# Kernel tuning notes

Hardware: AMD Instinct MI355X
Metric: run time of the kernel (lower is better)

The kernel has to match this reference:

```python
import jax, jax.numpy as jnp
import numpy as np

L1 = 1536
L2 = 15
L3 = 64
COUNT = 8
B = 16384


def setup_inputs() -> dict:
    key = jax.random.key(0)
    ks = jax.random.split(key, 10)
    d_in = 2 * L1 // 2  # 1536
    s1 = 1.0 / np.sqrt(d_in)
    s2 = 1.0 / np.sqrt(2 * L2)
    s3 = 1.0 / np.sqrt(L3)
    return {
        "x": jax.random.normal(ks[0], (B, d_in), dtype=jnp.float32),
        "ls_indices": jax.random.randint(ks[1], (B,), 0, COUNT, dtype=jnp.int32),
        "W1": jax.random.uniform(ks[2], (COUNT * (L2 + 1), d_in), jnp.float32, -s1, s1),
        "b1": jax.random.uniform(ks[3], (COUNT * (L2 + 1),), jnp.float32, -s1, s1),
        "Wf": jax.random.uniform(ks[4], (L2 + 1, d_in), jnp.float32, -s1, s1),
        "bf": jax.random.uniform(ks[5], (L2 + 1,), jnp.float32, -s1, s1),
        "W2": jax.random.uniform(ks[6], (COUNT * L3, 2 * L2), jnp.float32, -s2, s2),
        "b2": jax.random.uniform(ks[7], (COUNT * L3,), jnp.float32, -s2, s2),
        "Wo": jax.random.uniform(ks[8], (COUNT, L3), jnp.float32, -s3, s3),
        "bo": jax.random.uniform(ks[9], (COUNT,), jnp.float32, -s3, s3),
    }


def reference(x, ls_indices, W1, b1, Wf, bf, W2, b2, Wo, bo):
    count = Wo.shape[0]
    n = x.shape[0]
    idx = ls_indices[:, None, None]  # [B,1,1] selects the per-sample stack

    # l1: all stacks, then gather selected stack row per sample
    l1s = (x @ W1.T + b1).reshape(n, count, L2 + 1)          # [B, count, 16]
    l1f = x @ Wf.T + bf                                       # [B, 16]
    l1c = jnp.take_along_axis(l1s, idx, axis=1)[:, 0]         # [B, 16]

    l1c_, l1c_out = l1c[:, :L2], l1c[:, L2:]                  # [B,15], [B,1]
    l1f_, l1f_out = l1f[:, :L2], l1f[:, L2:]
    l1x = l1c_ + l1f_
    # squared-clipped-ReLU concat: [pow(x,2)*127/128, x] clamped to [0,1]
    l1x = jnp.clip(jnp.concatenate([l1x * l1x * (127.0 / 128.0), l1x], axis=1), 0.0, 1.0)  # [B,30]

    l2s = (l1x @ W2.T + b2).reshape(n, count, L3)             # [B, count, 64]
    l2c = jnp.take_along_axis(l2s, idx, axis=1)[:, 0]         # [B, 64]
    l2x = jnp.clip(l2c, 0.0, 1.0)

    l3s = (l2x @ Wo.T + bo).reshape(n, count, 1)              # [B, count, 1]
    l3c = jnp.take_along_axis(l3s, idx, axis=1)[:, 0]         # [B, 1]
    return l3c + l1f_out + l1c_out
```

## Files before the change

kernel.cpp:

```cpp
#include <hip/hip_runtime.h>
#include <hip/hip_bf16.h>
#include <stdint.h>

#define L1DIM 1536
#define NOUT  144
#define BK    64
#define MTILE 32
#define NCHUNK16 1152

typedef __bf16 bf16;
typedef __bf16 bf16x8 __attribute__((ext_vector_type(8)));
typedef float  floatx4 __attribute__((ext_vector_type(4)));

__global__ void pack_weights(const float* __restrict__ W1,
                             const float* __restrict__ Wf,
                             bf16* __restrict__ pw) {
    int t = blockIdx.x * blockDim.x + threadIdx.x;
    if (t >= 192 * NOUT) return;
    int o = t / NOUT;
    int n = t % NOUT;
    const float* src = (n < 128) ? (W1 + (size_t)n * L1DIM + o * 8)
                                 : (Wf + (size_t)(n - 128) * L1DIM + o * 8);
    bf16* dst = pw + (size_t)t * 8;
#pragma unroll
    for (int j = 0; j < 8; j++) dst[j] = (bf16)src[j];
}

__device__ __forceinline__ void gload_lds16(const void* g, void* l) {
    __builtin_amdgcn_global_load_lds(
        (const __attribute__((address_space(1))) void*)g,
        (__attribute__((address_space(3))) void*)l, 16, 0, 0);
}

__global__ __launch_bounds__(256) void layerstacks_main(
    const float* __restrict__ x, const int* __restrict__ lsidx,
    const bf16* __restrict__ pw,
    const float* __restrict__ b1, const float* __restrict__ bf_,
    const float* __restrict__ W2, const float* __restrict__ b2,
    const float* __restrict__ Wo, const float* __restrict__ bo,
    float* __restrict__ out)
{
    __shared__ bf16  lb[8 * NOUT * 8];
    __shared__ float ep[MTILE][148];

    const int tid  = threadIdx.x;
    const int wv   = tid >> 6;
    const int ln   = tid & 63;
    const int quad = ln >> 4;
    const int lm   = ln & 15;

    const int R0  = blockIdx.x * MTILE;
    const int ms  = wv & 1;
    const int nh  = wv >> 1;
    const int nt0 = nh ? 5 : 0;
    const int ntn = nh ? 4 : 5;

    const float* xrow = x + (size_t)(R0 + ms * 16 + lm) * L1DIM;

    floatx4 acc[5];
#pragma unroll
    for (int i = 0; i < 5; i++) acc[i] = (floatx4){0.f, 0.f, 0.f, 0.f};

    for (int ki = 0; ki < L1DIM / BK; ki++) {
        const int k0 = ki * BK;
        __syncthreads();
        {
            const bf16* src = pw + (size_t)(k0 / 8) * NOUT * 8;
            for (int base = wv * 64; base < NCHUNK16; base += 256) {
                gload_lds16(src + (size_t)(base + ln) * 8, &lb[(size_t)base * 8 + ln * 8]);
            }
        }
        float4 a0 = *(const float4*)(xrow + k0 + quad * 8);
        float4 a1 = *(const float4*)(xrow + k0 + quad * 8 + 4);
        float4 a2 = *(const float4*)(xrow + k0 + 32 + quad * 8);
        float4 a3 = *(const float4*)(xrow + k0 + 32 + quad * 8 + 4);
        bf16x8 af0, af1;
        {
            float t0[8] = {a0.x, a0.y, a0.z, a0.w, a1.x, a1.y, a1.z, a1.w};
            float t1[8] = {a2.x, a2.y, a2.z, a2.w, a3.x, a3.y, a3.z, a3.w};
#pragma unroll
            for (int j = 0; j < 8; j++) { af0[j] = (bf16)t0[j]; af1[j] = (bf16)t1[j]; }
        }
        __syncthreads();
#pragma unroll
        for (int t = 0; t < 5; t++) {
            if (t < ntn) {
                const int nt = nt0 + t;
                bf16x8 bf0 = *(const bf16x8*)&lb[((quad)     * NOUT + nt * 16 + lm) * 8];
                bf16x8 bf1 = *(const bf16x8*)&lb[((4 + quad) * NOUT + nt * 16 + lm) * 8];
                acc[t] = __builtin_amdgcn_mfma_f32_16x16x32_bf16(af0, bf0, acc[t], 0, 0, 0);
                acc[t] = __builtin_amdgcn_mfma_f32_16x16x32_bf16(af1, bf1, acc[t], 0, 0, 0);
            }
        }
    }

#pragma unroll
    for (int t = 0; t < 5; t++) {
        if (t < ntn) {
            const int nt = nt0 + t;
#pragma unroll
            for (int r = 0; r < 4; r++)
                ep[ms * 16 + quad * 4 + r][nt * 16 + lm] = acc[t][r];
        }
    }
    __syncthreads();

    const int er   = tid >> 3;
    const int sub  = tid & 7;
    const int grow = R0 + er;
    const int bkt  = lsidx[grow];

    const float l1c15 = ep[er][bkt * 16 + 15] + b1[bkt * 16 + 15];
    const float l1f15 = ep[er][128 + 15] + bf_[15];

    float l1x[30];
#pragma unroll
    for (int j = 0; j < 15; j++) {
        float tj = (ep[er][bkt * 16 + j] + b1[bkt * 16 + j])
                 + (ep[er][128 + j]      + bf_[j]);
        float sq = tj * tj * (127.0f / 128.0f);
        l1x[j]      = fminf(fmaxf(sq, 0.f), 1.f);
        l1x[15 + j] = fminf(fmaxf(tj, 0.f), 1.f);
    }

    float part = 0.f;
#pragma unroll
    for (int o = 0; o < 8; o++) {
        const int oi = bkt * 64 + sub * 8 + o;
        const float2* wrow = (const float2*)(W2 + oi * 30);
        float a = b2[oi];
#pragma unroll
        for (int j2 = 0; j2 < 15; j2++) {
            float2 w = wrow[j2];
            a += l1x[2 * j2] * w.x + l1x[2 * j2 + 1] * w.y;
        }
        a = fminf(fmaxf(a, 0.f), 1.f);
        part += a * Wo[oi];
    }
    part += __shfl_xor(part, 1);
    part += __shfl_xor(part, 2);
    part += __shfl_xor(part, 4);
    if (sub == 0) out[grow] = part + bo[bkt] + l1c15 + l1f15;
}

extern "C" void kernel_launch(void* const* d_in, const int* in_sizes, int n_in,
                              void* d_out, int out_size, void* d_ws, size_t ws_size,
                              hipStream_t stream) {
    const float* x   = (const float*)d_in[0];
    const int*   idx = (const int*)  d_in[1];
    const float* W1  = (const float*)d_in[2];
    const float* b1  = (const float*)d_in[3];
    const float* Wf  = (const float*)d_in[4];
    const float* bf  = (const float*)d_in[5];
    const float* W2  = (const float*)d_in[6];
    const float* b2  = (const float*)d_in[7];
    const float* Wo  = (const float*)d_in[8];
    const float* bo  = (const float*)d_in[9];
    float* out = (float*)d_out;
    bf16*  pw  = (bf16*)d_ws;

    pack_weights<<<dim3((192 * NOUT + 255) / 256), dim3(256), 0, stream>>>(W1, Wf, pw);
    layerstacks_main<<<dim3(16384 / MTILE), dim3(256), 0, stream>>>(
        x, idx, pw, b1, bf, W2, b2, Wo, bo, out);
}
```

Measured before the change: 186.6 us.

## Split K across waves, read packed weights from global, drop LDS staging

The main GEMM loop no longer stages weight tiles into LDS with per-iteration barriers. Each wave pair now takes half of the K dimension and computes all 9 N-tiles, reading B fragments straight from global/L2. The two halves are reduced through the epilogue shared buffer. The pack kernel now reads float4 and writes vectors with a transposed thread mapping for coalesced reads. The trade is more global/L2 weight traffic per block and more accumulator registers, in exchange for removing the barriers and the LDS copy.

```diff
diff --git a/kernel.cpp b/kernel.cpp
--- a/kernel.cpp
+++ b/kernel.cpp
@@ -4,9 +4,8 @@
 
 #define L1DIM 1536
 #define NOUT  144
-#define BK    64
 #define MTILE 32
-#define NCHUNK16 1152
+#define KHALF 24
 
 typedef __bf16 bf16;
 typedef __bf16 bf16x8 __attribute__((ext_vector_type(8)));
@@ -16,20 +15,17 @@
                              const float* __restrict__ Wf,
                              bf16* __restrict__ pw) {
     int t = blockIdx.x * blockDim.x + threadIdx.x;
-    if (t >= 192 * NOUT) return;
-    int o = t / NOUT;
-    int n = t % NOUT;
+    if (t >= NOUT * 192) return;
+    int n = t / 192;
+    int o = t % 192;
     const float* src = (n < 128) ? (W1 + (size_t)n * L1DIM + o * 8)
                                  : (Wf + (size_t)(n - 128) * L1DIM + o * 8);
-    bf16* dst = pw + (size_t)t * 8;
-#pragma unroll
-    for (int j = 0; j < 8; j++) dst[j] = (bf16)src[j];
-}
-
-__device__ __forceinline__ void gload_lds16(const void* g, void* l) {
-    __builtin_amdgcn_global_load_lds(
-        (const __attribute__((address_space(1))) void*)g,
-        (__attribute__((address_space(3))) void*)l, 16, 0, 0);
+    float4 s0 = ((const float4*)src)[0];
+    float4 s1 = ((const float4*)src)[1];
+    bf16x8 v;
+    v[0] = (bf16)s0.x; v[1] = (bf16)s0.y; v[2] = (bf16)s0.z; v[3] = (bf16)s0.w;
+    v[4] = (bf16)s1.x; v[5] = (bf16)s1.y; v[6] = (bf16)s1.z; v[7] = (bf16)s1.w;
+    *(bf16x8*)(pw + ((size_t)o * NOUT + n) * 8) = v;
 }
 
 __global__ __launch_bounds__(256) void layerstacks_main(
@@ -40,7 +36,6 @@
     const float* __restrict__ Wo, const float* __restrict__ bo,
     float* __restrict__ out)
 {
-    __shared__ bf16  lb[8 * NOUT * 8];
     __shared__ float ep[MTILE][148];
 
     const int tid  = threadIdx.x;
@@ -49,59 +44,47 @@
     const int quad = ln >> 4;
     const int lm   = ln & 15;
 
-    const int R0  = blockIdx.x * MTILE;
-    const int ms  = wv & 1;
-    const int nh  = wv >> 1;
-    const int nt0 = nh ? 5 : 0;
-    const int ntn = nh ? 4 : 5;
+    const int R0 = blockIdx.x * MTILE;
+    const int ms = wv & 1;
+    const int kh = wv >> 1;
 
-    const float* xrow = x + (size_t)(R0 + ms * 16 + lm) * L1DIM;
+    const float* xrow = x + (size_t)(R0 + ms * 16 + lm) * L1DIM + kh * (KHALF * 32);
+    const bf16* pwb = pw + ((size_t)(kh * 96 + quad) * NOUT + lm) * 8;
 
-    floatx4 acc[5];
+    floatx4 acc[9];
 #pragma unroll
-    for (int i = 0; i < 5; i++) acc[i] = (floatx4){0.f, 0.f, 0.f, 0.f};
+    for (int i = 0; i < 9; i++) acc[i] = (floatx4){0.f, 0.f, 0.f, 0.f};
 
-    for (int ki = 0; ki < L1DIM / BK; ki++) {
-        const int k0 = ki * BK;
-        __syncthreads();
-        {
-            const bf16* src = pw + (size_t)(k0 / 8) * NOUT * 8;
-            for (int base = wv * 64; base < NCHUNK16; base += 256) {
-                gload_lds16(src + (size_t)(base + ln) * 8, &lb[(size_t)base * 8 + ln * 8]);
-            }
-        }
-        float4 a0 = *(const float4*)(xrow + k0 + quad * 8);
-        float4 a1 = *(const float4*)(xrow + k0 + quad * 8 + 4);
-        float4 a2 = *(const float4*)(xrow + k0 + 32 + quad * 8);
-        float4 a3 = *(const float4*)(xrow + k0 + 32 + quad * 8 + 4);
-        bf16x8 af0, af1;
-        {
-            float t0[8] = {a0.x, a0.y, a0.z, a0.w, a1.x, a1.y, a1.z, a1.w};
-            float t1[8] = {a2.x, a2.y, a2.z, a2.w, a3.x, a3.y, a3.z, a3.w};
+#pragma unroll 3
+    for (int s = 0; s < KHALF; s++) {
+        float4 a0 = *(const float4*)(xrow + s * 32 + quad * 8);
+        float4 a1 = *(const float4*)(xrow + s * 32 + quad * 8 + 4);
+        bf16x8 af;
+        af[0] = (bf16)a0.x; af[1] = (bf16)a0.y; af[2] = (bf16)a0.z; af[3] = (bf16)a0.w;
+        af[4] = (bf16)a1.x; af[5] = (bf16)a1.y; af[6] = (bf16)a1.z; af[7] = (bf16)a1.w;
+
+        const bf16* bb = pwb + (size_t)s * 4 * NOUT * 8;
 #pragma unroll
-            for (int j = 0; j < 8; j++) { af0[j] = (bf16)t0[j]; af1[j] = (bf16)t1[j]; }
-        }
-        __syncthreads();
-#pragma unroll
-        for (int t = 0; t < 5; t++) {
-            if (t < ntn) {
-                const int nt = nt0 + t;
-                bf16x8 bf0 = *(const bf16x8*)&lb[((quad)     * NOUT + nt * 16 + lm) * 8];
-                bf16x8 bf1 = *(const bf16x8*)&lb[((4 + quad) * NOUT + nt * 16 + lm) * 8];
-                acc[t] = __builtin_amdgcn_mfma_f32_16x16x32_bf16(af0, bf0, acc[t], 0, 0, 0);
-                acc[t] = __builtin_amdgcn_mfma_f32_16x16x32_bf16(af1, bf1, acc[t], 0, 0, 0);
-            }
+        for (int nt = 0; nt < 9; nt++) {
+            bf16x8 bfrag = *(const bf16x8*)(bb + nt * 16 * 8);
+            acc[nt] = __builtin_amdgcn_mfma_f32_16x16x32_bf16(af, bfrag, acc[nt], 0, 0, 0);
         }
     }
 
+    if (kh == 0) {
 #pragma unroll
-    for (int t = 0; t < 5; t++) {
-        if (t < ntn) {
-            const int nt = nt0 + t;
+        for (int nt = 0; nt < 9; nt++)
 #pragma unroll
             for (int r = 0; r < 4; r++)
-                ep[ms * 16 + quad * 4 + r][nt * 16 + lm] = acc[t][r];
-        }
+                ep[ms * 16 + quad * 4 + r][nt * 16 + lm] = acc[nt][r];
+    }
+    __syncthreads();
+    if (kh == 1) {
+#pragma unroll
+        for (int nt = 0; nt < 9; nt++)
+#pragma unroll
+            for (int r = 0; r < 4; r++)
+                ep[ms * 16 + quad * 4 + r][nt * 16 + lm] += acc[nt][r];
     }
     __syncthreads();
 
@@ -159,7 +142,7 @@
     float* out = (float*)d_out;
     bf16*  pw  = (bf16*)d_ws;
 
-    pack_weights<<<dim3((192 * NOUT + 255) / 256), dim3(256), 0, stream>>>(W1, Wf, pw);
+    pack_weights<<<dim3((NOUT * 192 + 255) / 256), dim3(256), 0, stream>>>(W1, Wf, pw);
     layerstacks_main<<<dim3(16384 / MTILE), dim3(256), 0, stream>>>(
         x, idx, pw, b1, bf, W2, b2, Wo, bo, out);
 }
```

After: 225.1 us. +20.7%, slower.

## Double-buffer weight tiles in LDS, prefetch x, and double rows per block

Applied to the files above, without the earlier changes.

The main GEMM loop now double-buffers the packed weight tile in LDS and prefetches the next x slice into registers while the MFMAs work on the current one. This leaves one barrier per iteration instead of two and overlaps global loads with compute. The block grows to 512 threads covering 64 rows, so each weight tile loaded into LDS is reused across twice as many rows. The pack kernel is also reworked to read source rows contiguously with float4 loads and write 16-byte vectors. The cost is double the LDS for weights and a larger epilogue buffer, which may lower occupancy.

```diff
diff --git a/kernel.cpp b/kernel.cpp
--- a/kernel.cpp
+++ b/kernel.cpp
@@ -4,8 +4,9 @@
 
 #define L1DIM 1536
 #define NOUT  144
+#define MTILE 64
 #define BK    64
-#define MTILE 32
+#define NITER (L1DIM / BK)
 #define NCHUNK16 1152
 
 typedef __bf16 bf16;
@@ -16,14 +17,17 @@
                              const float* __restrict__ Wf,
                              bf16* __restrict__ pw) {
     int t = blockIdx.x * blockDim.x + threadIdx.x;
-    if (t >= 192 * NOUT) return;
-    int o = t / NOUT;
-    int n = t % NOUT;
+    if (t >= NOUT * 192) return;
+    int n = t / 192;
+    int o = t % 192;
     const float* src = (n < 128) ? (W1 + (size_t)n * L1DIM + o * 8)
                                  : (Wf + (size_t)(n - 128) * L1DIM + o * 8);
-    bf16* dst = pw + (size_t)t * 8;
-#pragma unroll
-    for (int j = 0; j < 8; j++) dst[j] = (bf16)src[j];
+    float4 s0 = ((const float4*)src)[0];
+    float4 s1 = ((const float4*)src)[1];
+    bf16x8 v;
+    v[0] = (bf16)s0.x; v[1] = (bf16)s0.y; v[2] = (bf16)s0.z; v[3] = (bf16)s0.w;
+    v[4] = (bf16)s1.x; v[5] = (bf16)s1.y; v[6] = (bf16)s1.z; v[7] = (bf16)s1.w;
+    *(bf16x8*)(pw + ((size_t)o * NOUT + n) * 8) = v;
 }
 
 __device__ __forceinline__ void gload_lds16(const void* g, void* l) {
@@ -32,7 +36,7 @@
         (__attribute__((address_space(3))) void*)l, 16, 0, 0);
 }
 
-__global__ __launch_bounds__(256) void layerstacks_main(
+__global__ __launch_bounds__(512) void layerstacks_main(
     const float* __restrict__ x, const int* __restrict__ lsidx,
     const bf16* __restrict__ pw,
     const float* __restrict__ b1, const float* __restrict__ bf_,
@@ -40,7 +44,7 @@
     const float* __restrict__ Wo, const float* __restrict__ bo,
     float* __restrict__ out)
 {
-    __shared__ bf16  lb[8 * NOUT * 8];
+    __shared__ bf16  lb[2][8 * NOUT * 8];
     __shared__ float ep[MTILE][148];
 
     const int tid  = threadIdx.x;
@@ -50,48 +54,61 @@
     const int lm   = ln & 15;
 
     const int R0  = blockIdx.x * MTILE;
-    const int ms  = wv & 1;
-    const int nh  = wv >> 1;
+    const int rg  = wv & 3;
+    const int nh  = wv >> 2;
     const int nt0 = nh ? 5 : 0;
     const int ntn = nh ? 4 : 5;
 
-    const float* xrow = x + (size_t)(R0 + ms * 16 + lm) * L1DIM;
+    const float* xrow = x + (size_t)(R0 + rg * 16 + lm) * L1DIM;
 
     floatx4 acc[5];
 #pragma unroll
     for (int i = 0; i < 5; i++) acc[i] = (floatx4){0.f, 0.f, 0.f, 0.f};
 
-    for (int ki = 0; ki < L1DIM / BK; ki++) {
-        const int k0 = ki * BK;
-        __syncthreads();
-        {
-            const bf16* src = pw + (size_t)(k0 / 8) * NOUT * 8;
-            for (int base = wv * 64; base < NCHUNK16; base += 256) {
-                gload_lds16(src + (size_t)(base + ln) * 8, &lb[(size_t)base * 8 + ln * 8]);
+#pragma unroll
+    for (int c = 0; c < 3; c++) {
+        int ch = tid + c * 512;
+        if (ch < NCHUNK16) gload_lds16(pw + (size_t)ch * 8, &lb[0][(size_t)ch * 8]);
+    }
+    float4 a0 = *(const float4*)(xrow + quad * 8);
+    float4 a1 = *(const float4*)(xrow + quad * 8 + 4);
+    float4 a2 = *(const float4*)(xrow + 32 + quad * 8);
+    float4 a3 = *(const float4*)(xrow + 32 + quad * 8 + 4);
+    __syncthreads();
+
+    for (int ki = 0; ki < NITER; ki++) {
+        const int cur = ki & 1;
+        if (ki < NITER - 1) {
+            const bf16* src = pw + (size_t)(ki + 1) * 8 * NOUT * 8;
+#pragma unroll
+            for (int c = 0; c < 3; c++) {
+                int ch = tid + c * 512;
+                if (ch < NCHUNK16) gload_lds16(src + (size_t)ch * 8, &lb[cur ^ 1][(size_t)ch * 8]);
             }
         }
-        float4 a0 = *(const float4*)(xrow + k0 + quad * 8);
-        float4 a1 = *(const float4*)(xrow + k0 + quad * 8 + 4);
-        float4 a2 = *(const float4*)(xrow + k0 + 32 + quad * 8);
-        float4 a3 = *(const float4*)(xrow + k0 + 32 + quad * 8 + 4);
         bf16x8 af0, af1;
-        {
-            float t0[8] = {a0.x, a0.y, a0.z, a0.w, a1.x, a1.y, a1.z, a1.w};
-            float t1[8] = {a2.x, a2.y, a2.z, a2.w, a3.x, a3.y, a3.z, a3.w};
-#pragma unroll
-            for (int j = 0; j < 8; j++) { af0[j] = (bf16)t0[j]; af1[j] = (bf16)t1[j]; }
+        af0[0] = (bf16)a0.x; af0[1] = (bf16)a0.y; af0[2] = (bf16)a0.z; af0[3] = (bf16)a0.w;
+        af0[4] = (bf16)a1.x; af0[5] = (bf16)a1.y; af0[6] = (bf16)a1.z; af0[7] = (bf16)a1.w;
+        af1[0] = (bf16)a2.x; af1[1] = (bf16)a2.y; af1[2] = (bf16)a2.z; af1[3] = (bf16)a2.w;
+        af1[4] = (bf16)a3.x; af1[5] = (bf16)a3.y; af1[6] = (bf16)a3.z; af1[7] = (bf16)a3.w;
+        if (ki < NITER - 1) {
+            const float* xk = xrow + (ki + 1) * BK;
+            a0 = *(const float4*)(xk + quad * 8);
+            a1 = *(const float4*)(xk + quad * 8 + 4);
+            a2 = *(const float4*)(xk + 32 + quad * 8);
+            a3 = *(const float4*)(xk + 32 + quad * 8 + 4);
         }
-        __syncthreads();
 #pragma unroll
         for (int t = 0; t < 5; t++) {
             if (t < ntn) {
                 const int nt = nt0 + t;
-                bf16x8 bf0 = *(const bf16x8*)&lb[((quad)     * NOUT + nt * 16 + lm) * 8];
-                bf16x8 bf1 = *(const bf16x8*)&lb[((4 + quad) * NOUT + nt * 16 + lm) * 8];
+                bf16x8 bf0 = *(const bf16x8*)&lb[cur][((quad)     * NOUT + nt * 16 + lm) * 8];
+                bf16x8 bf1 = *(const bf16x8*)&lb[cur][((4 + quad) * NOUT + nt * 16 + lm) * 8];
                 acc[t] = __builtin_amdgcn_mfma_f32_16x16x32_bf16(af0, bf0, acc[t], 0, 0, 0);
                 acc[t] = __builtin_amdgcn_mfma_f32_16x16x32_bf16(af1, bf1, acc[t], 0, 0, 0);
             }
         }
+        __syncthreads();
     }
 
 #pragma unroll
@@ -100,7 +117,7 @@
             const int nt = nt0 + t;
 #pragma unroll
             for (int r = 0; r < 4; r++)
-                ep[ms * 16 + quad * 4 + r][nt * 16 + lm] = acc[t][r];
+                ep[rg * 16 + quad * 4 + r][nt * 16 + lm] = acc[t][r];
         }
     }
     __syncthreads();
@@ -159,7 +176,7 @@
     float* out = (float*)d_out;
     bf16*  pw  = (bf16*)d_ws;
 
-    pack_weights<<<dim3((192 * NOUT + 255) / 256), dim3(256), 0, stream>>>(W1, Wf, pw);
-    layerstacks_main<<<dim3(16384 / MTILE), dim3(256), 0, stream>>>(
+    pack_weights<<<dim3((NOUT * 192 + 255) / 256), dim3(256), 0, stream>>>(W1, Wf, pw);
+    layerstacks_main<<<dim3(16384 / MTILE), dim3(512), 0, stream>>>(
         x, idx, pw, b1, bf, W2, b2, Wo, bo, out);
 }
```

Result: no change. 183.7 us (-1.5%).
